# Performance work log

Measured on AMD Instinct MI355X. Metric: run time of the kernel, lower is better.

The kernel has to match this reference:

```python
import jax, jax.numpy as jnp
import numpy as np

DROP_P = 0.5

def setup_inputs() -> dict:
    key = jax.random.key(0)
    k_x, k_q, k_k, k_v = jax.random.split(key, 4)
    T, d_in, d_out = 4096, 1024, 1024
    x = jax.random.normal(k_x, (T, d_in), dtype=jnp.float32)
    # torch nn.Linear weights are [d_out, d_in]; init scale ~ 1/sqrt(d_in)
    s = 1.0 / np.sqrt(d_in)
    W_query = jax.random.uniform(k_q, (d_out, d_in), jnp.float32, -s, s)
    W_key = jax.random.uniform(k_k, (d_out, d_in), jnp.float32, -s, s)
    W_value = jax.random.uniform(k_v, (d_out, d_in), jnp.float32, -s, s)
    return {"x": x, "W_query": W_query, "W_key": W_key, "W_value": W_value}


def reference(x, W_query, W_key, W_value):
    # QKV projections (y = x @ W.T, matching torch Linear)
    queries = x @ W_query.T          # [T, d]
    keys = x @ W_key.T               # [T, d]
    # values = x @ W_value.T  -> feeds only the unused context_vec; dead code omitted
    d = keys.shape[-1]
    T = x.shape[0]
    attn_scores = queries @ keys.T   # [T, T]
    attn_weights = jax.nn.softmax(attn_scores / jnp.sqrt(jnp.float32(d)), axis=-1)
    # post-softmax causal masking + row renormalization (as in source)
    row = jnp.arange(T)
    causal = (row[:, None] >= row[None, :]).astype(attn_weights.dtype)  # tril of ones
    masked = attn_weights * causal
    masked_norm = masked / jnp.sum(masked, axis=-1, keepdims=True)
    # dropout(p=0.5), train mode, fixed seed
    keep = jax.random.bernoulli(jax.random.key(123), 1.0 - DROP_P, masked_norm.shape)
    return jnp.where(keep, masked_norm / (1.0 - DROP_P), 0.0)
```

## Files before the change

kernel.cpp:

```cpp
#include <hip/hip_runtime.h>
#include <hip/hip_bf16.h>


using bf16   = __bf16;
using bf16x8 = __attribute__((ext_vector_type(8))) __bf16;
using bf16x4 = __attribute__((ext_vector_type(4))) __bf16;
using f32x4  = __attribute__((ext_vector_type(4))) float;

constexpr int Tdim = 4096;
constexpr int Ddim = 1024;

__global__ __launch_bounds__(256) void k_cast_bf16(const float* __restrict__ in,
                                                   bf16* __restrict__ out, int n4) {
  int i = blockIdx.x * 256 + threadIdx.x;
  if (i >= n4) return;
  f32x4 v = reinterpret_cast<const f32x4*>(in)[i];
  bf16x4 o;
  o[0] = (bf16)v[0]; o[1] = (bf16)v[1]; o[2] = (bf16)v[2]; o[3] = (bf16)v[3];
  reinterpret_cast<bf16x4*>(out)[i] = o;
}

__global__ __launch_bounds__(256) void k_tcast(const float* __restrict__ q,
                                               const float* __restrict__ k,
                                               bf16* __restrict__ qt,
                                               bf16* __restrict__ kt) {
  const float* in = blockIdx.z ? k : q;
  bf16* out = blockIdx.z ? kt : qt;
  __shared__ float t[32][33];
  const int tx = threadIdx.x & 31;
  const int ty = threadIdx.x >> 5;
  const int r0 = blockIdx.y * 32;
  const int c0 = blockIdx.x * 32;
#pragma unroll
  for (int r = 0; r < 4; ++r)
    t[ty * 4 + r][tx] = in[(r0 + ty * 4 + r) * Ddim + c0 + tx];
  __syncthreads();
#pragma unroll
  for (int r = 0; r < 4; ++r)
    out[(c0 + ty * 4 + r) * Ddim + r0 + tx] = (bf16)t[tx][ty * 4 + r];
}

__global__ __launch_bounds__(256) void k_redcast(const float* __restrict__ p,
                                                 bf16* __restrict__ g) {
  const int i = blockIdx.x * 256 + threadIdx.x;
  f32x4 a = reinterpret_cast<const f32x4*>(p)[i];
  f32x4 b = reinterpret_cast<const f32x4*>(p + (1 << 20))[i];
  f32x4 c = reinterpret_cast<const f32x4*>(p + (2 << 20))[i];
  f32x4 d = reinterpret_cast<const f32x4*>(p + (3 << 20))[i];
  f32x4 s = a + b + c + d;
  bf16x4 o;
  o[0] = (bf16)s[0]; o[1] = (bf16)s[1]; o[2] = (bf16)s[2]; o[3] = (bf16)s[3];
  reinterpret_cast<bf16x4*>(g)[i] = o;
}

__device__ __forceinline__ void gll16(const bf16* g, bf16* l) {
  __builtin_amdgcn_global_load_lds(
      (const __attribute__((address_space(1))) void*)g,
      (__attribute__((address_space(3))) void*)l, 16, 0, 0);
}

template<int BM, int OUTF32>
__global__ __launch_bounds__(512)
void k_gemm(const bf16* __restrict__ A, const bf16* __restrict__ B,
            void* __restrict__ Cv, int N, int lda, int ldb, int kLen,
            long cZs, int causal) {
  constexpr int LPT = (BM == 256) ? 4 : 3;
  constexpr int FM  = BM / 32;
  __shared__ __align__(16) bf16 As[4][BM * 32];
  __shared__ __align__(16) bf16 Bs[4][256 * 32];

  int bx = blockIdx.x;
  {
    const int cpx = gridDim.x >> 3;
    bx = (bx & 7) * cpx + (bx >> 3);
  }
  const int nbn = N >> 8;
  const int bm = bx / nbn;
  const int bn = bx - bm * nbn;
  if (causal && bn > bm) return;

  const int tid  = threadIdx.x;
  const int lane = tid & 63;
  const int wid  = tid >> 6;
  const int wrr  = (wid >> 2) * (BM / 2);
  const int wcc  = (wid & 3) * 64;
  const int fr   = lane & 15;
  const int g8   = (lane >> 4) * 8;

  f32x4 acc[FM][4];
#pragma unroll
  for (int i = 0; i < FM; ++i)
#pragma unroll
    for (int j = 0; j < 4; ++j) acc[i][j] = (f32x4){0.f, 0.f, 0.f, 0.f};

  const bf16* Ag = A + (long)bm * BM * lda;
  const bf16* Bg = B + (long)bn * 256 * ldb;
  const int k0 = blockIdx.y * kLen;
  const int nt = kLen >> 5;

  const bf16* pa0 = Ag + (long)(tid >> 2) * lda + (tid & 3) * 8;
  const bf16* pa1 = pa0 + (long)128 * lda;
  const bf16* pb0 = Bg + (long)(tid >> 2) * ldb + (tid & 3) * 8;
  const bf16* pb1 = pb0 + (long)128 * ldb;

  auto stageA = [&](int buf, int kt) {
    gll16(pa0 + kt, &As[buf][tid * 8]);
    if constexpr (BM == 256) gll16(pa1 + kt, &As[buf][(tid + 512) * 8]);
  };
  auto stageB = [&](int buf, int kt) {
    gll16(pb0 + kt, &Bs[buf][tid * 8]);
    gll16(pb1 + kt, &Bs[buf][(tid + 512) * 8]);
  };

  stageA(0, k0);      stageB(0, k0);
  stageA(1, k0 + 32); stageB(1, k0 + 32);
  stageA(2, k0 + 64); stageB(2, k0 + 64);

  for (int t = 0; t < nt; ++t) {
    const int buf = t & 3;
    if (t < nt - 2) {
      if constexpr (BM == 256) asm volatile("s_waitcnt vmcnt(8)" ::: "memory");
      else                     asm volatile("s_waitcnt vmcnt(6)" ::: "memory");
    } else if (t == nt - 2) {
      if constexpr (BM == 256) asm volatile("s_waitcnt vmcnt(4)" ::: "memory");
      else                     asm volatile("s_waitcnt vmcnt(3)" ::: "memory");
    } else {
      asm volatile("s_waitcnt vmcnt(0)" ::: "memory");
    }
    __builtin_amdgcn_sched_barrier(0);
    __builtin_amdgcn_s_barrier();
    __builtin_amdgcn_sched_barrier(0);

    const int ks = k0 + (t + 3) * 32;
    const bool more = (t + 3) < nt;
    const int nbuf = (t + 3) & 3;

    bf16x8 av[4], bv[4];
#pragma unroll
    for (int n = 0; n < 4; ++n)
      bv[n] = *reinterpret_cast<const bf16x8*>(&Bs[buf][(wcc + n * 16 + fr) * 32 + g8]);
#pragma unroll
    for (int m = 0; m < 4; ++m)
      av[m] = *reinterpret_cast<const bf16x8*>(&As[buf][(wrr + m * 16 + fr) * 32 + g8]);
    if (more) stageA(nbuf, ks);
    __builtin_amdgcn_s_setprio(1);
#pragma unroll
    for (int m = 0; m < 4; ++m)
#pragma unroll
      for (int n = 0; n < 4; ++n)
        acc[m][n] = __builtin_amdgcn_mfma_f32_16x16x32_bf16(av[m], bv[n], acc[m][n], 0, 0, 0);
    __builtin_amdgcn_s_setprio(0);

    if constexpr (BM == 256) {
#pragma unroll
      for (int m = 0; m < 4; ++m)
        av[m] = *reinterpret_cast<const bf16x8*>(&As[buf][(wrr + (m + 4) * 16 + fr) * 32 + g8]);
      if (more) stageB(nbuf, ks);
      __builtin_amdgcn_s_setprio(1);
#pragma unroll
      for (int m = 0; m < 4; ++m)
#pragma unroll
        for (int n = 0; n < 4; ++n)
          acc[m + 4][n] = __builtin_amdgcn_mfma_f32_16x16x32_bf16(av[m], bv[n], acc[m + 4][n], 0, 0, 0);
      __builtin_amdgcn_s_setprio(0);
    } else {
      if (more) stageB(nbuf, ks);
    }
  }

  const int crow = (lane >> 4) * 4;
  const int ccol = lane & 15;
#pragma unroll
  for (int m = 0; m < FM; ++m)
#pragma unroll
    for (int n = 0; n < 4; ++n)
#pragma unroll
      for (int j = 0; j < 4; ++j) {
        const long row = (long)bm * BM + wrr + m * 16 + crow + j;
        const long col = (long)bn * 256 + wcc + n * 16 + ccol;
        const float v = acc[m][n][j];
        if (OUTF32) ((float*)Cv + (long)blockIdx.y * cZs)[row * N + col] = v;
        else        ((bf16*)Cv)[row * N + col] = (bf16)v;
      }
}

__device__ __forceinline__ unsigned rotl32(unsigned v, int d) {
  return (v << d) | (v >> (32 - d));
}
__device__ __forceinline__ void threefry_123(unsigned x0, unsigned x1,
                                             unsigned& o0, unsigned& o1) {
  const unsigned ks0 = 0u, ks1 = 123u;
  const unsigned ks2 = 0x1BD11BDAu ^ ks0 ^ ks1;
  x0 += ks0; x1 += ks1;
#define TF_R4(a, b, c, d)                                   \
  x0 += x1; x1 = rotl32(x1, a); x1 ^= x0;                   \
  x0 += x1; x1 = rotl32(x1, b); x1 ^= x0;                   \
  x0 += x1; x1 = rotl32(x1, c); x1 ^= x0;                   \
  x0 += x1; x1 = rotl32(x1, d); x1 ^= x0;
  TF_R4(13, 15, 26, 6);  x0 += ks1; x1 += ks2 + 1u;
  TF_R4(17, 29, 16, 24); x0 += ks2; x1 += ks0 + 2u;
  TF_R4(13, 15, 26, 6);  x0 += ks0; x1 += ks1 + 3u;
  TF_R4(17, 29, 16, 24); x0 += ks1; x1 += ks2 + 4u;
  TF_R4(13, 15, 26, 6);  x0 += ks2; x1 += ks0 + 5u;
#undef TF_R4
  o0 = x0; o1 = x1;
}
__device__ __forceinline__ bool keep_bit(unsigned i) {
  unsigned o0, o1;
  threefry_123(0u, i, o0, o1);
  return ((o0 ^ o1) & 0x80000000u) == 0u;
}

__global__ __launch_bounds__(256) void k_softmax_drop(float* __restrict__ S) {
  const int b  = blockIdx.x;
  const int r0 = b, r1 = b + (Tdim / 2);
  const int tid = threadIdx.x;
  const int cb  = tid * 16;
  __shared__ float redA[4], redB[4];

  float* row0 = S + (long)r0 * Tdim;
  float* row1 = S + (long)r1 * Tdim;

  f32x4 v1[4], v0[4];
  float lm0 = -3.0e38f, lm1 = -3.0e38f;
#pragma unroll
  for (int i = 0; i < 4; ++i) {
    const int c = cb + i * 4;
    f32x4 v = (c <= r1) ? *reinterpret_cast<const f32x4*>(row1 + c)
                        : (f32x4){0.f, 0.f, 0.f, 0.f};
#pragma unroll
    for (int l = 0; l < 4; ++l) {
      if (c + l > r1) v[l] = -3.0e38f;
      lm1 = fmaxf(lm1, v[l]);
    }
    v1[i] = v;
  }
  if (tid < 128) {
#pragma unroll
    for (int i = 0; i < 4; ++i) {
      const int c = cb + i * 4;
      f32x4 v = (c <= r0) ? *reinterpret_cast<const f32x4*>(row0 + c)
                          : (f32x4){0.f, 0.f, 0.f, 0.f};
#pragma unroll
      for (int l = 0; l < 4; ++l) {
        if (c + l > r0) v[l] = -3.0e38f;
        lm0 = fmaxf(lm0, v[l]);
      }
      v0[i] = v;
    }
  }
#pragma unroll
  for (int o = 32; o; o >>= 1) {
    lm0 = fmaxf(lm0, __shfl_xor(lm0, o));
    lm1 = fmaxf(lm1, __shfl_xor(lm1, o));
  }
  if ((tid & 63) == 0) { redA[tid >> 6] = lm0; redB[tid >> 6] = lm1; }
  __syncthreads();
  const float m0 = fmaxf(fmaxf(redA[0], redA[1]), fmaxf(redA[2], redA[3]));
  const float m1 = fmaxf(fmaxf(redB[0], redB[1]), fmaxf(redB[2], redB[3]));
  __syncthreads();

  constexpr float SC = 1.0f / 32.0f;
  float ls0 = 0.f, ls1 = 0.f;
#pragma unroll
  for (int i = 0; i < 4; ++i) {
#pragma unroll
    for (int l = 0; l < 4; ++l) {
      const int c = cb + i * 4 + l;
      float e = 0.f;
      if (c <= r1) { e = __expf((v1[i][l] - m1) * SC); ls1 += e; }
      v1[i][l] = e;
    }
  }
  if (tid < 128) {
#pragma unroll
    for (int i = 0; i < 4; ++i) {
#pragma unroll
      for (int l = 0; l < 4; ++l) {
        const int c = cb + i * 4 + l;
        float e = 0.f;
        if (c <= r0) { e = __expf((v0[i][l] - m0) * SC); ls0 += e; }
        v0[i][l] = e;
      }
    }
  }
#pragma unroll
  for (int o = 32; o; o >>= 1) { ls0 += __shfl_xor(ls0, o); ls1 += __shfl_xor(ls1, o); }
  if ((tid & 63) == 0) { redA[tid >> 6] = ls0; redB[tid >> 6] = ls1; }
  __syncthreads();
  const float inv0 = 2.0f / (redA[0] + redA[1] + redA[2] + redA[3]);
  const float inv1 = 2.0f / (redB[0] + redB[1] + redB[2] + redB[3]);

#pragma unroll
  for (int i = 0; i < 4; ++i) {
    const int c = cb + i * 4;
    f32x4 o1v = {0.f, 0.f, 0.f, 0.f};
#pragma unroll
    for (int l = 0; l < 4; ++l) {
      const int cc = c + l;
      if (cc <= r1 && keep_bit((unsigned)(r1 * Tdim + cc))) o1v[l] = v1[i][l] * inv1;
    }
    *reinterpret_cast<f32x4*>(row1 + c) = o1v;
    f32x4 o0v = {0.f, 0.f, 0.f, 0.f};
    if (tid < 128) {
#pragma unroll
      for (int l = 0; l < 4; ++l) {
        const int cc = c + l;
        if (cc <= r0 && keep_bit((unsigned)(r0 * Tdim + cc))) o0v[l] = v0[i][l] * inv0;
      }
    }
    *reinterpret_cast<f32x4*>(row0 + c) = o0v;
  }
}

extern "C" void kernel_launch(void* const* d_in, const int* in_sizes, int n_in,
                              void* d_out, int out_size, void* d_ws, size_t ws_size,
                              hipStream_t stream) {
  const float* x  = (const float*)d_in[0];
  const float* Wq = (const float*)d_in[1];
  const float* Wk = (const float*)d_in[2];
  float* S = (float*)d_out;
  char* ws = (char*)d_ws;
  bf16*  xb = (bf16*)(ws);
  bf16*  qt = (bf16*)(ws + (8l  << 20));
  bf16*  kt = (bf16*)(ws + (10l << 20));
  float* Wp = (float*)(ws + (12l << 20));
  bf16*  G  = (bf16*)(ws + (28l << 20));
  bf16*  P  = (bf16*)(ws + (30l << 20));

  k_cast_bf16<<<(Tdim * Ddim / 4) / 256, 256, 0, stream>>>(x, xb, Tdim * Ddim / 4);
  k_tcast<<<dim3(32, 32, 2), 256, 0, stream>>>(Wq, Wk, qt, kt);

  k_gemm<128, 1><<<dim3(32, 4), 512, 0, stream>>>(kt, qt, (void*)Wp, Ddim, Ddim,
                                                  Ddim, Ddim / 4, 1l << 20, 0);
  k_redcast<<<(Ddim * Ddim / 4) / 256, 256, 0, stream>>>(Wp, G);

  k_gemm<128, 0><<<dim3(128, 1), 512, 0, stream>>>(xb, G, (void*)P, Ddim, Ddim,
                                                   Ddim, Ddim, 0, 0);
  k_gemm<256, 1><<<dim3(256, 1), 512, 0, stream>>>(P, xb, (void*)S, Tdim, Ddim,
                                                   Ddim, Ddim, 0, 1);

  k_softmax_drop<<<Tdim / 2, 256, 0, stream>>>(S);
}
```

Baseline: 195.0 us.

## Add triangular-grid specialized score GEMM with 4-phase pipelined LDS schedule

```diff
diff --git a/kernel.cpp b/kernel.cpp
--- a/kernel.cpp
+++ b/kernel.cpp
@@ -1,5 +1,6 @@
 #include <hip/hip_runtime.h>
 #include <hip/hip_bf16.h>
+#include <math.h>
 
 
 using bf16   = __bf16;
@@ -64,7 +65,6 @@
 void k_gemm(const bf16* __restrict__ A, const bf16* __restrict__ B,
             void* __restrict__ Cv, int N, int lda, int ldb, int kLen,
             long cZs, int causal) {
-  constexpr int LPT = (BM == 256) ? 4 : 3;
   constexpr int FM  = BM / 32;
   __shared__ __align__(16) bf16 As[4][BM * 32];
   __shared__ __align__(16) bf16 Bs[4][256 * 32];
@@ -182,6 +182,186 @@
         if (OUTF32) ((float*)Cv + (long)blockIdx.y * cZs)[row * N + col] = v;
         else        ((bf16*)Cv)[row * N + col] = (bf16)v;
       }
+}
+
+__global__ __launch_bounds__(512, 2)
+void k_gemm_s(const bf16* __restrict__ A, const bf16* __restrict__ B,
+              float* __restrict__ C) {
+  __shared__ __align__(16) bf16 As[2][2][128 * 64];
+  __shared__ __align__(16) bf16 Bs[2][2][128 * 64];
+
+  int swz = (blockIdx.x & 7) * 17 + (blockIdx.x >> 3);
+  int bm = (int)((sqrtf(8.f * swz + 1.f) - 1.f) * 0.5f);
+  while ((bm + 1) * (bm + 2) / 2 <= swz) ++bm;
+  while (bm * (bm + 1) / 2 > swz) --bm;
+  const int bn = swz - bm * (bm + 1) / 2;
+
+  const int tid  = threadIdx.x;
+  const int lane = tid & 63;
+  const int wid  = tid >> 6;
+  const int wm   = wid >> 2, wn = wid & 3;
+  const int fr   = lane & 15;
+  const int lh   = lane >> 4;
+
+  const bf16* Ag = A + (long)bm * 256 * Ddim;
+  const bf16* Bg = B + (long)bn * 256 * Ddim;
+
+  const int r1 = tid >> 3,         c1 = ((tid & 7) ^ (r1 & 7)) * 8;
+  const int r2 = (tid + 512) >> 3, c2 = ((tid & 7) ^ (r2 & 7)) * 8;
+  const bf16* pA0a = Ag + (long)r1 * Ddim + c1;
+  const bf16* pA0b = Ag + (long)r2 * Ddim + c2;
+  const bf16* pA1a = pA0a + (long)128 * Ddim;
+  const bf16* pA1b = pA0b + (long)128 * Ddim;
+  const bf16* pB0a = Bg + (long)r1 * Ddim + c1;
+  const bf16* pB0b = Bg + (long)r2 * Ddim + c2;
+  const bf16* pB1a = pB0a + (long)128 * Ddim;
+  const bf16* pB1b = pB0b + (long)128 * Ddim;
+  const int d1 = tid * 8, d2 = (tid + 512) * 8;
+
+  auto stage = [&](int buf, int which, int kt) {
+    switch (which) {
+      case 0: gll16(pA0a + kt, &As[buf][0][d1]); gll16(pA0b + kt, &As[buf][0][d2]); break;
+      case 1: gll16(pB0a + kt, &Bs[buf][0][d1]); gll16(pB0b + kt, &Bs[buf][0][d2]); break;
+      case 2: gll16(pB1a + kt, &Bs[buf][1][d1]); gll16(pB1b + kt, &Bs[buf][1][d2]); break;
+      case 3: gll16(pA1a + kt, &As[buf][1][d1]); gll16(pA1b + kt, &As[buf][1][d2]); break;
+    }
+  };
+  auto rd = [&](const bf16* half, int row, int chunk) -> bf16x8 {
+    return *reinterpret_cast<const bf16x8*>(half + row * 64 + ((chunk ^ (row & 7)) * 8));
+  };
+
+  f32x4 acc[8][4];
+#pragma unroll
+  for (int i = 0; i < 8; ++i)
+#pragma unroll
+    for (int j = 0; j < 4; ++j) acc[i][j] = (f32x4){0.f, 0.f, 0.f, 0.f};
+
+  const int nt = Ddim / 64;
+  stage(0, 0, 0); stage(0, 1, 0); stage(0, 2, 0); stage(0, 3, 0);
+  asm volatile("s_waitcnt vmcnt(4)" ::: "memory");
+  __builtin_amdgcn_sched_barrier(0);
+  __builtin_amdgcn_s_barrier();
+
+  bf16x8 av[8], bv0[4], bv1[4];
+  for (int t = 0; t < nt; ++t) {
+    const int buf = t & 1, nbuf = buf ^ 1;
+    const int kt = (t + 1) * 64;
+    const bool pf = (t + 1) < nt;
+    const bf16* Ah0 = &As[buf][0][0];
+    const bf16* Ah1 = &As[buf][1][0];
+    const bf16* Bh0 = &Bs[buf][0][0];
+    const bf16* Bh1 = &Bs[buf][1][0];
+
+#pragma unroll
+    for (int m = 0; m < 4; ++m) {
+      const int row = wm * 64 + m * 16 + fr;
+      av[m * 2]     = rd(Ah0, row, lh);
+      av[m * 2 + 1] = rd(Ah0, row, 4 + lh);
+    }
+#pragma unroll
+    for (int n = 0; n < 2; ++n) {
+      const int row = wn * 32 + n * 16 + fr;
+      bv0[n * 2]     = rd(Bh0, row, lh);
+      bv0[n * 2 + 1] = rd(Bh0, row, 4 + lh);
+    }
+    if (pf) stage(nbuf, 0, kt);
+    __builtin_amdgcn_s_barrier();
+    asm volatile("s_waitcnt lgkmcnt(0)" ::: "memory");
+    __builtin_amdgcn_sched_barrier(0);
+    __builtin_amdgcn_s_setprio(1);
+#pragma unroll
+    for (int m = 0; m < 4; ++m)
+#pragma unroll
+      for (int n = 0; n < 2; ++n) {
+        acc[m][n] = __builtin_amdgcn_mfma_f32_16x16x32_bf16(av[m*2],   bv0[n*2],   acc[m][n], 0, 0, 0);
+        acc[m][n] = __builtin_amdgcn_mfma_f32_16x16x32_bf16(av[m*2+1], bv0[n*2+1], acc[m][n], 0, 0, 0);
+      }
+    __builtin_amdgcn_s_setprio(0);
+    if (pf) asm volatile("s_waitcnt vmcnt(4)" ::: "memory");
+    else    asm volatile("s_waitcnt vmcnt(2)" ::: "memory");
+    __builtin_amdgcn_sched_barrier(0);
+    __builtin_amdgcn_s_barrier();
+
+#pragma unroll
+    for (int n = 0; n < 2; ++n) {
+      const int row = wn * 32 + n * 16 + fr;
+      bv1[n * 2]     = rd(Bh1, row, lh);
+      bv1[n * 2 + 1] = rd(Bh1, row, 4 + lh);
+    }
+    if (pf) stage(nbuf, 1, kt);
+    __builtin_amdgcn_s_barrier();
+    asm volatile("s_waitcnt lgkmcnt(0)" ::: "memory");
+    __builtin_amdgcn_sched_barrier(0);
+    __builtin_amdgcn_s_setprio(1);
+#pragma unroll
+    for (int m = 0; m < 4; ++m)
+#pragma unroll
+      for (int n = 0; n < 2; ++n) {
+        acc[m][2+n] = __builtin_amdgcn_mfma_f32_16x16x32_bf16(av[m*2],   bv1[n*2],   acc[m][2+n], 0, 0, 0);
+        acc[m][2+n] = __builtin_amdgcn_mfma_f32_16x16x32_bf16(av[m*2+1], bv1[n*2+1], acc[m][2+n], 0, 0, 0);
+      }
+    __builtin_amdgcn_s_setprio(0);
+    if (pf) asm volatile("s_waitcnt vmcnt(4)" ::: "memory");
+    else    asm volatile("s_waitcnt vmcnt(0)" ::: "memory");
+    __builtin_amdgcn_sched_barrier(0);
+    __builtin_amdgcn_s_barrier();
+
+#pragma unroll
+    for (int m = 0; m < 4; ++m) {
+      const int row = wm * 64 + m * 16 + fr;
+      av[m * 2]     = rd(Ah1, row, lh);
+      av[m * 2 + 1] = rd(Ah1, row, 4 + lh);
+    }
+    if (pf) stage(nbuf, 2, kt);
+    __builtin_amdgcn_s_barrier();
+    asm volatile("s_waitcnt lgkmcnt(0)" ::: "memory");
+    __builtin_amdgcn_sched_barrier(0);
+    __builtin_amdgcn_s_setprio(1);
+#pragma unroll
+    for (int m = 0; m < 4; ++m)
+#pragma unroll
+      for (int n = 0; n < 2; ++n) {
+        acc[4+m][n] = __builtin_amdgcn_mfma_f32_16x16x32_bf16(av[m*2],   bv0[n*2],   acc[4+m][n], 0, 0, 0);
+        acc[4+m][n] = __builtin_amdgcn_mfma_f32_16x16x32_bf16(av[m*2+1], bv0[n*2+1], acc[4+m][n], 0, 0, 0);
+      }
+    __builtin_amdgcn_s_setprio(0);
+    __builtin_amdgcn_s_barrier();
+
+    if (pf) stage(nbuf, 3, kt);
+    __builtin_amdgcn_s_barrier();
+    __builtin_amdgcn_sched_barrier(0);
+    __builtin_amdgcn_s_setprio(1);
+#pragma unroll
+    for (int m = 0; m < 4; ++m)
+#pragma unroll
+      for (int n = 0; n < 2; ++n) {
+        acc[4+m][2+n] = __builtin_amdgcn_mfma_f32_16x16x32_bf16(av[m*2],   bv1[n*2],   acc[4+m][2+n], 0, 0, 0);
+        acc[4+m][2+n] = __builtin_amdgcn_mfma_f32_16x16x32_bf16(av[m*2+1], bv1[n*2+1], acc[4+m][2+n], 0, 0, 0);
+      }
+    __builtin_amdgcn_s_setprio(0);
+    if (pf) {
+      asm volatile("s_waitcnt vmcnt(4)" ::: "memory");
+      __builtin_amdgcn_sched_barrier(0);
+    }
+    __builtin_amdgcn_s_barrier();
+  }
+
+  const int crow = (lane >> 4) * 4;
+  const int ccol = lane & 15;
+#pragma unroll
+  for (int qm = 0; qm < 2; ++qm)
+#pragma unroll
+    for (int m = 0; m < 4; ++m)
+#pragma unroll
+      for (int qn = 0; qn < 2; ++qn)
+#pragma unroll
+        for (int n = 0; n < 2; ++n)
+#pragma unroll
+          for (int j = 0; j < 4; ++j) {
+            const long row = (long)bm * 256 + qm * 128 + wm * 64 + m * 16 + crow + j;
+            const long col = (long)bn * 256 + qn * 128 + wn * 32 + n * 16 + ccol;
+            C[row * Tdim + col] = acc[qm * 4 + m][qn * 2 + n][j];
+          }
 }
 
 __device__ __forceinline__ unsigned rotl32(unsigned v, int d) {
@@ -213,7 +393,7 @@
 
 __global__ __launch_bounds__(256) void k_softmax_drop(float* __restrict__ S) {
   const int b  = blockIdx.x;
-  const int r0 = b, r1 = b + (Tdim / 2);
+  const int r0 = b, r1 = Tdim - 1 - b;
   const int tid = threadIdx.x;
   const int cb  = tid * 16;
   __shared__ float redA[4], redB[4];
@@ -235,19 +415,17 @@
     }
     v1[i] = v;
   }
-  if (tid < 128) {
-#pragma unroll
-    for (int i = 0; i < 4; ++i) {
-      const int c = cb + i * 4;
-      f32x4 v = (c <= r0) ? *reinterpret_cast<const f32x4*>(row0 + c)
-                          : (f32x4){0.f, 0.f, 0.f, 0.f};
-#pragma unroll
-      for (int l = 0; l < 4; ++l) {
-        if (c + l > r0) v[l] = -3.0e38f;
-        lm0 = fmaxf(lm0, v[l]);
-      }
-      v0[i] = v;
-    }
+#pragma unroll
+  for (int i = 0; i < 4; ++i) {
+    const int c = cb + i * 4;
+    f32x4 v = (c <= r0) ? *reinterpret_cast<const f32x4*>(row0 + c)
+                        : (f32x4){0.f, 0.f, 0.f, 0.f};
+#pragma unroll
+    for (int l = 0; l < 4; ++l) {
+      if (c + l > r0) v[l] = -3.0e38f;
+      lm0 = fmaxf(lm0, v[l]);
+    }
+    v0[i] = v;
   }
 #pragma unroll
   for (int o = 32; o; o >>= 1) {
@@ -270,18 +448,9 @@
       float e = 0.f;
       if (c <= r1) { e = __expf((v1[i][l] - m1) * SC); ls1 += e; }
       v1[i][l] = e;
-    }
-  }
-  if (tid < 128) {
-#pragma unroll
-    for (int i = 0; i < 4; ++i) {
-#pragma unroll
-      for (int l = 0; l < 4; ++l) {
-        const int c = cb + i * 4 + l;
-        float e = 0.f;
-        if (c <= r0) { e = __expf((v0[i][l] - m0) * SC); ls0 += e; }
-        v0[i][l] = e;
-      }
+      float e0 = 0.f;
+      if (c <= r0) { e0 = __expf((v0[i][l] - m0) * SC); ls0 += e0; }
+      v0[i][l] = e0;
     }
   }
 #pragma unroll
@@ -302,12 +471,10 @@
     }
     *reinterpret_cast<f32x4*>(row1 + c) = o1v;
     f32x4 o0v = {0.f, 0.f, 0.f, 0.f};
-    if (tid < 128) {
-#pragma unroll
-      for (int l = 0; l < 4; ++l) {
-        const int cc = c + l;
-        if (cc <= r0 && keep_bit((unsigned)(r0 * Tdim + cc))) o0v[l] = v0[i][l] * inv0;
-      }
+#pragma unroll
+    for (int l = 0; l < 4; ++l) {
+      const int cc = c + l;
+      if (cc <= r0 && keep_bit((unsigned)(r0 * Tdim + cc))) o0v[l] = v0[i][l] * inv0;
     }
     *reinterpret_cast<f32x4*>(row0 + c) = o0v;
   }
@@ -337,8 +504,7 @@
 
   k_gemm<128, 0><<<dim3(128, 1), 512, 0, stream>>>(xb, G, (void*)P, Ddim, Ddim,
                                                    Ddim, Ddim, 0, 0);
-  k_gemm<256, 1><<<dim3(256, 1), 512, 0, stream>>>(P, xb, (void*)S, Tdim, Ddim,
-                                                   Ddim, Ddim, 0, 1);
+  k_gemm_s<<<136, 512, 0, stream>>>(P, xb, S);
 
   k_softmax_drop<<<Tdim / 2, 256, 0, stream>>>(S);
 }
```

Result: faster. 188.6 us (-3.3%).
